# Optimization experiments

Hardware: AMD Instinct MI355X
Metric: run time of the kernel (lower is better)

Reference implementation:

```python
import jax, jax.numpy as jnp
import numpy as np

B, F0, D = 2048, 39, 16
LAYER_SIZES = [128, 128, 128]  # split_half=True -> field_nums [39, 64, 64]


def setup_inputs() -> dict:
    key = jax.random.key(0)
    ks = jax.random.split(key, 1 + 2 * len(LAYER_SIZES))
    inputs = jax.random.normal(ks[0], (B, F0, D), dtype=jnp.float32)
    out = {"inputs": inputs}
    field_nums = [F0]
    for i, size in enumerate(LAYER_SIZES):
        fk = field_nums[-1]
        fan_in = F0 * fk  # conv1d filter fan-in (kernel width 1)
        scale = np.sqrt(2.0 / (fan_in + size)).astype(np.float32)  # glorot
        # filter stored as [F0, Fk, size]; TF flat index is h0*Fk + hk
        out[f"w{i}"] = jax.random.normal(ks[1 + 2 * i], (F0, fk, size), dtype=jnp.float32) * scale
        out[f"b{i}"] = jnp.zeros((size,), dtype=jnp.float32)
        field_nums.append(size // 2)  # split_half=True
    return out


def reference(inputs, w0, w1, w2, b0, b1, b2):
    # CIN: per-embedding-dim outer product of x0 and x_{k-1}, then 1x1 conv
    # (shared dense over field pairs). Fused here as a single einsum per layer.
    x0 = inputs  # [B, F0, D]
    xk = inputs  # [B, Fk, D]
    params = [(w0, b0), (w1, b1), (w2, b2)]
    n_layers = len(params)
    direct = []
    for idx, (W, b) in enumerate(params):
        # out[b, s, d] = sum_{h,k} x0[b,h,d] * xk[b,k,d] * W[h,k,s]
        z = jnp.einsum('bhd,bkd,hks->bsd', x0, xk, W) + b[None, :, None]
        z = jax.nn.relu(z)  # activation='relu'
        if idx != n_layers - 1:
            half = z.shape[1] // 2  # split_half: first half feeds next layer
            xk = z[:, :half, :]
            direct.append(z[:, half:, :])
        else:
            direct.append(z)
    logit = jnp.sum(jnp.concatenate(direct, axis=1), axis=-1)  # [B, 64+64+128]
    return logit
```

## Files before the change

### kernel.cpp

```cpp
#include <hip/hip_runtime.h>
#include <stdint.h>
#include <stddef.h>

#define F0N  39
#define SN   128
#define NB   8
#define X0TS 45
#define XKTS 72
#define WBLK 8192
#define NHB2 234

typedef __attribute__((ext_vector_type(8))) short short8;
typedef __attribute__((ext_vector_type(4))) float floatx4;

__device__ __forceinline__ uint16_t f2bf(float f) {
  uint32_t u = __float_as_uint(f);
  u += 0x7fffu + ((u >> 16) & 1u);
  return (uint16_t)(u >> 16);
}

__global__ __launch_bounds__(256) void cin_prepass(
    const float* __restrict__ w0, const float* __restrict__ w1,
    const float* __restrict__ w2, uint16_t* __restrict__ wt) {
  __shared__ float T[32 * 132];
  const int bc = blockIdx.x;
  const int ch = bc & 1;
  const int lh = bc >> 1;
  const int L = lh / F0N;
  const int h = lh - L * F0N;
  const float* W = (L == 0) ? w0 : ((L == 1) ? w1 : w2);
  const int fk = (L == 0) ? 39 : 64;
  const int tid = threadIdx.x;

  for (int e = tid; e < 4096; e += 256) {
    int kc = e >> 7, s = e & 127;
    int k = ch * 32 + kc;
    T[kc * 132 + s] = (k < fk) ? W[(h * fk + k) * SN + s] : 0.0f;
  }
  __syncthreads();
  uint32_t* dst = (uint32_t*)(wt + (size_t)lh * WBLK);
  for (int i = tid; i < 2048; i += 256) {
    int st = i >> 8, w = i & 255;
    int ln = w >> 2, jp = w & 3;
    int quad = ln >> 4, l16 = ln & 15;
    int k0 = quad * 8 + jp * 2;
    int s = st * 16 + l16;
    dst[(size_t)(st * 2 + ch) * 256 + w] =
        (uint32_t)f2bf(T[k0 * 132 + s]) | ((uint32_t)f2bf(T[(k0 + 1) * 132 + s]) << 16);
  }
}

__global__ __launch_bounds__(1024) void cin_main(
    const float* __restrict__ x,
    const float* __restrict__ bias0, const float* __restrict__ bias1,
    const float* __restrict__ bias2,
    const uint16_t* __restrict__ wt,
    float* __restrict__ out) {

  __shared__ __align__(16) float    X0T[NB * 16 * X0TS];
  __shared__ __align__(16) uint16_t XKT[NB * 16 * XKTS];

  const int tid  = threadIdx.x;
  const int lane = tid & 63;
  const int wave = tid >> 6;
  const int st   = wave >> 1;
  const int bg   = wave & 1;
  const int l16  = lane & 15;
  const int quad = lane >> 4;
  const int bbase = blockIdx.x * NB;

  {
    float* p = X0T;
#pragma unroll
    for (int i = 0; i < 6; i++) { int e = tid + 1024 * i; if (e < NB * 16 * X0TS) p[e] = 0.f; }
    uint32_t* q = (uint32_t*)XKT;
#pragma unroll
    for (int i = 0; i < 5; i++) { int e = tid + 1024 * i; if (e < NB * 16 * XKTS / 2) q[e] = 0u; }
  }
  __syncthreads();

#pragma unroll
  for (int it = 0; it < 5; ++it) {
    int e = tid + it * 1024;
    if (e < NB * F0N * 16) {
      float v = x[(size_t)bbase * (F0N * 16) + e];
      int d = e & 15, p = e >> 4;
      int b = p / F0N, h = p - b * F0N;
      X0T[(b * 16 + d) * X0TS + h] = v;
    }
  }
  __syncthreads();

  if (tid < 512) {
    int b = tid >> 6, d = (tid >> 2) & 15, kg = tid & 3;
    const float* src = &X0T[(b * 16 + d) * X0TS];
    uint32_t* drow = (uint32_t*)&XKT[(b * 16 + d) * XKTS + kg * 16];
#pragma unroll
    for (int i2 = 0; i2 < 8; i2++) {
      int k0 = kg * 16 + i2 * 2;
      uint32_t lo = (k0 < 39)     ? (uint32_t)f2bf(src[k0])     : 0u;
      uint32_t hi = (k0 + 1 < 39) ? (uint32_t)f2bf(src[k0 + 1]) : 0u;
      drow[i2] = lo | (hi << 16);
    }
  }
  __syncthreads();

  const int stlane = st * 1024 + lane * 8;

  short8 Wc0 = *(const short8*)(wt + stlane);
  short8 Wc1 = *(const short8*)(wt + stlane + 512);

  int ih = 0;
#pragma unroll 1
  for (int L = 0; L < 3; ++L) {
    short8 Bf0[4], Bf1[4];
#pragma unroll
    for (int bi = 0; bi < 4; ++bi) {
      const uint16_t* r = XKT + ((bg * 4 + bi) * 16 + l16) * XKTS + quad * 8;
      Bf0[bi] = *(const short8*)r;
      Bf1[bi] = *(const short8*)(r + 32);
    }

    floatx4 z[4] = {};
    const floatx4 zero4 = {0.f, 0.f, 0.f, 0.f};

#pragma unroll 3
    for (int h = 0; h < 39; ++h, ++ih) {
      int ihn = ih + 1;
      if (ihn > 116) ihn = 116;
      const uint16_t* wb = wt + (size_t)ihn * WBLK + stlane;
      short8 Wn0 = *(const short8*)(wb);
      short8 Wn1 = *(const short8*)(wb + 512);

      float xs[4];
#pragma unroll
      for (int bi = 0; bi < 4; ++bi)
        xs[bi] = X0T[((bg * 4 + bi) * 16 + l16) * X0TS + h];

#pragma unroll
      for (int bi = 0; bi < 4; ++bi) {
        floatx4 y = __builtin_amdgcn_mfma_f32_16x16x32_bf16(Wc0, Bf0[bi], zero4, 0, 0, 0);
        y = __builtin_amdgcn_mfma_f32_16x16x32_bf16(Wc1, Bf1[bi], y, 0, 0, 0);
#pragma unroll
        for (int r = 0; r < 4; ++r) z[bi][r] += xs[bi] * y[r];
      }
      Wc0 = Wn0;
      Wc1 = Wn1;
    }

    const float* bp = (L == 0) ? bias0 : ((L == 1) ? bias1 : bias2);
#pragma unroll
    for (int bi = 0; bi < 4; ++bi) {
      const int b = bg * 4 + bi;
#pragma unroll
      for (int r = 0; r < 4; ++r) {
        float t = fmaxf(z[bi][r] + bp[st * 16 + quad * 4 + r], 0.f);
        if (L < 2 && st < 4)
          XKT[(b * 16 + l16) * XKTS + st * 16 + quad * 4 + r] = f2bf(t);
        float s4 = t;
        s4 += __shfl_xor(s4, 1);
        s4 += __shfl_xor(s4, 2);
        s4 += __shfl_xor(s4, 4);
        s4 += __shfl_xor(s4, 8);
        if (l16 == 0) {
          int s = st * 16 + quad * 4 + r;
          if (L == 2)       out[(size_t)(bbase + b) * 256 + 128 + s] = s4;
          else if (s >= 64) out[(size_t)(bbase + b) * 256 + L * 64 + (s - 64)] = s4;
        }
      }
    }
    if (L < 2) __syncthreads();
  }
}

extern "C" void kernel_launch(void* const* d_in, const int* in_sizes, int n_in,
                              void* d_out, int out_size, void* d_ws, size_t ws_size,
                              hipStream_t stream) {
  (void)in_sizes; (void)n_in; (void)out_size; (void)ws_size;
  const float* x  = (const float*)d_in[0];
  const float* w0 = (const float*)d_in[1];
  const float* b0 = (const float*)d_in[2];
  const float* w1 = (const float*)d_in[3];
  const float* b1 = (const float*)d_in[4];
  const float* w2 = (const float*)d_in[5];
  const float* b2 = (const float*)d_in[6];
  uint16_t* wt    = (uint16_t*)d_ws;

  cin_prepass<<<NHB2, 256, 0, stream>>>(w0, w1, w2, wt);
  cin_main<<<256, 1024, 0, stream>>>(x, b0, b1, b2, wt, (float*)d_out);
}
```

Before: 138.0 us.

## Premultiply x0 into bf16 operand tiles and accumulate directly in MFMA

Instead of running two MFMAs per h into a zero accumulator and then scaling by x0 on the CUDA cores, each h step builds a bf16 tile U = x0[h]*xk in shared memory, double-buffered across h, and feeds it to MFMA that accumulates straight into z. The goal is to remove the per-h scalar FMA epilogue and keep the reduction over h inside the matrix cores. In exchange it adds shared-memory tile construction, LDS reads, a __syncthreads per h, and an extra bf16 rounding of the product. The xk layout is changed to fit the MFMA operand format, and dynamic shared memory is enlarged to hold the two U buffers.

Result: slower. 149.8 us (+8.5%).

```diff
diff --git a/kernel.cpp b/kernel.cpp
--- a/kernel.cpp
+++ b/kernel.cpp
@@ -6,17 +6,36 @@
 #define SN   128
 #define NB   8
 #define X0TS 45
-#define XKTS 72
 #define WBLK 8192
 #define NHB2 234
+#define X0T_BYTES 23040
+#define XKT_OFF   23040
+#define U0_OFF    39424
+#define U1_OFF    55808
+#define SMEM_TOTAL 72192
 
 typedef __attribute__((ext_vector_type(8))) short short8;
 typedef __attribute__((ext_vector_type(4))) float floatx4;
+typedef __attribute__((ext_vector_type(8))) float floatx8;
+typedef __attribute__((ext_vector_type(8))) __bf16 bf16x8;
 
 __device__ __forceinline__ uint16_t f2bf(float f) {
   uint32_t u = __float_as_uint(f);
   u += 0x7fffu + ((u >> 16) & 1u);
   return (uint16_t)(u >> 16);
+}
+
+__device__ __forceinline__ void build_u(const float* X0T, const uint16_t* XKT,
+                                        uint16_t* dst, int xrow, int toff, int hn) {
+  float xs = X0T[xrow + hn];
+  short8 xkv = *(const short8*)(XKT + toff);
+  bf16x8 xb = __builtin_bit_cast(bf16x8, xkv);
+  floatx8 xf = __builtin_convertvector(xb, floatx8);
+  floatx8 pf;
+#pragma unroll
+  for (int j = 0; j < 8; ++j) pf[j] = xf[j] * xs;
+  *(short8*)(dst + toff) =
+      __builtin_bit_cast(short8, __builtin_convertvector(pf, bf16x8));
 }
 
 __global__ __launch_bounds__(256) void cin_prepass(
@@ -57,8 +76,11 @@
     const uint16_t* __restrict__ wt,
     float* __restrict__ out) {
 
-  __shared__ __align__(16) float    X0T[NB * 16 * X0TS];
-  __shared__ __align__(16) uint16_t XKT[NB * 16 * XKTS];
+  extern __shared__ __align__(16) char smem[];
+  float*    X0T = (float*)smem;
+  uint16_t* XKT = (uint16_t*)(smem + XKT_OFF);
+  uint16_t* U0  = (uint16_t*)(smem + U0_OFF);
+  uint16_t* U1  = (uint16_t*)(smem + U1_OFF);
 
   const int tid  = threadIdx.x;
   const int lane = tid & 63;
@@ -69,13 +91,12 @@
   const int quad = lane >> 4;
   const int bbase = blockIdx.x * NB;
 
+  const int xrow = ((tid >> 7) * 16 + (tid & 15)) * X0TS;
+  const int toff = tid * 8;
+
   {
-    float* p = X0T;
-#pragma unroll
-    for (int i = 0; i < 6; i++) { int e = tid + 1024 * i; if (e < NB * 16 * X0TS) p[e] = 0.f; }
-    uint32_t* q = (uint32_t*)XKT;
-#pragma unroll
-    for (int i = 0; i < 5; i++) { int e = tid + 1024 * i; if (e < NB * 16 * XKTS / 2) q[e] = 0u; }
+#pragma unroll
+    for (int i = 0; i < 6; i++) { int e = tid + 1024 * i; if (e < NB * 16 * X0TS) X0T[e] = 0.f; }
   }
   __syncthreads();
 
@@ -91,21 +112,20 @@
   }
   __syncthreads();
 
-  if (tid < 512) {
-    int b = tid >> 6, d = (tid >> 2) & 15, kg = tid & 3;
-    const float* src = &X0T[(b * 16 + d) * X0TS];
-    uint32_t* drow = (uint32_t*)&XKT[(b * 16 + d) * XKTS + kg * 16];
-#pragma unroll
-    for (int i2 = 0; i2 < 8; i2++) {
-      int k0 = kg * 16 + i2 * 2;
-      uint32_t lo = (k0 < 39)     ? (uint32_t)f2bf(src[k0])     : 0u;
-      uint32_t hi = (k0 + 1 < 39) ? (uint32_t)f2bf(src[k0 + 1]) : 0u;
-      drow[i2] = lo | (hi << 16);
-    }
+  {
+    int k8 = (tid >> 4) & 7;
+    uint16_t vals[8];
+#pragma unroll
+    for (int j = 0; j < 8; ++j) {
+      int k = k8 * 8 + j;
+      vals[j] = (k < F0N) ? f2bf(X0T[xrow + k]) : (uint16_t)0;
+    }
+    *(short8*)(XKT + toff) = *(short8*)vals;
   }
   __syncthreads();
 
   const int stlane = st * 1024 + lane * 8;
+  const int ulane = bg * 4096 + quad * 128 + l16 * 8;
 
   short8 Wc0 = *(const short8*)(wt + stlane);
   short8 Wc1 = *(const short8*)(wt + stlane + 512);
@@ -113,18 +133,15 @@
   int ih = 0;
 #pragma unroll 1
   for (int L = 0; L < 3; ++L) {
-    short8 Bf0[4], Bf1[4];
-#pragma unroll
-    for (int bi = 0; bi < 4; ++bi) {
-      const uint16_t* r = XKT + ((bg * 4 + bi) * 16 + l16) * XKTS + quad * 8;
-      Bf0[bi] = *(const short8*)r;
-      Bf1[bi] = *(const short8*)(r + 32);
-    }
+    uint16_t* ua  = U0;
+    uint16_t* ubn = U1;
+
+    build_u(X0T, XKT, ua, xrow, toff, 0);
+    __syncthreads();
 
     floatx4 z[4] = {};
-    const floatx4 zero4 = {0.f, 0.f, 0.f, 0.f};
-
-#pragma unroll 3
+
+#pragma unroll 1
     for (int h = 0; h < 39; ++h, ++ih) {
       int ihn = ih + 1;
       if (ihn > 116) ihn = 116;
@@ -132,20 +149,20 @@
       short8 Wn0 = *(const short8*)(wb);
       short8 Wn1 = *(const short8*)(wb + 512);
 
-      float xs[4];
-#pragma unroll
-      for (int bi = 0; bi < 4; ++bi)
-        xs[bi] = X0T[((bg * 4 + bi) * 16 + l16) * X0TS + h];
+      build_u(X0T, XKT, ubn, xrow, toff, h + 1);
 
 #pragma unroll
       for (int bi = 0; bi < 4; ++bi) {
-        floatx4 y = __builtin_amdgcn_mfma_f32_16x16x32_bf16(Wc0, Bf0[bi], zero4, 0, 0, 0);
-        y = __builtin_amdgcn_mfma_f32_16x16x32_bf16(Wc1, Bf1[bi], y, 0, 0, 0);
-#pragma unroll
-        for (int r = 0; r < 4; ++r) z[bi][r] += xs[bi] * y[r];
+        const uint16_t* ur = ua + ulane + bi * 1024;
+        short8 u0 = *(const short8*)(ur);
+        short8 u1 = *(const short8*)(ur + 512);
+        z[bi] = __builtin_amdgcn_mfma_f32_16x16x32_bf16(Wc0, u0, z[bi], 0, 0, 0);
+        z[bi] = __builtin_amdgcn_mfma_f32_16x16x32_bf16(Wc1, u1, z[bi], 0, 0, 0);
       }
       Wc0 = Wn0;
       Wc1 = Wn1;
+      { uint16_t* t = ua; ua = ubn; ubn = t; }
+      __syncthreads();
     }
 
     const float* bp = (L == 0) ? bias0 : ((L == 1) ? bias1 : bias2);
@@ -155,8 +172,10 @@
 #pragma unroll
       for (int r = 0; r < 4; ++r) {
         float t = fmaxf(z[bi][r] + bp[st * 16 + quad * 4 + r], 0.f);
-        if (L < 2 && st < 4)
-          XKT[(b * 16 + l16) * XKTS + st * 16 + quad * 4 + r] = f2bf(t);
+        if (L < 2 && st < 4) {
+          int s = st * 16 + quad * 4 + r;
+          XKT[((b * 8 + (s >> 3)) * 16 + l16) * 8 + (s & 7)] = f2bf(t);
+        }
         float s4 = t;
         s4 += __shfl_xor(s4, 1);
         s4 += __shfl_xor(s4, 2);
@@ -186,6 +205,14 @@
   const float* b2 = (const float*)d_in[6];
   uint16_t* wt    = (uint16_t*)d_ws;
 
+  static bool smem_cfg = false;
+  if (!smem_cfg) {
+    (void)hipFuncSetAttribute((const void*)cin_main,
+                              hipFuncAttributeMaxDynamicSharedMemorySize,
+                              SMEM_TOTAL);
+    smem_cfg = true;
+  }
+
   cin_prepass<<<NHB2, 256, 0, stream>>>(w0, w1, w2, wt);
-  cin_main<<<256, 1024, 0, stream>>>(x, b0, b1, b2, wt, (float*)d_out);
-}
+  cin_main<<<256, 1024, SMEM_TOTAL, stream>>>(x, b0, b1, b2, wt, (float*)d_out);
+}
```

## Software-pipeline MFMA results across h iterations and use packed FMA combine

Applied to the files above, without the earlier changes.

Restructures the h loop so the MFMA chain for iteration h is issued before the scaling/accumulation of iteration h-1's results. This hides MFMA latency behind the VALU combine step. It also switches the combine to 2-wide float vectors so the compiler can emit packed FMA, and hoists the X0T row offsets out of the loop. The cost is extra registers for the in-flight results, which could add pressure in a 1024-thread block.

New measurement: 142.2 us. 3.0% more time.

```diff
diff --git a/kernel.cpp b/kernel.cpp
--- a/kernel.cpp
+++ b/kernel.cpp
@@ -12,6 +12,7 @@
 
 typedef __attribute__((ext_vector_type(8))) short short8;
 typedef __attribute__((ext_vector_type(4))) float floatx4;
+typedef __attribute__((ext_vector_type(2))) float floatx2;
 
 __device__ __forceinline__ uint16_t f2bf(float f) {
   uint32_t u = __float_as_uint(f);
@@ -107,8 +108,25 @@
 
   const int stlane = st * 1024 + lane * 8;
 
+  int xoff[4];
+#pragma unroll
+  for (int bi = 0; bi < 4; ++bi)
+    xoff[bi] = ((bg * 4 + bi) * 16 + l16) * X0TS;
+
   short8 Wc0 = *(const short8*)(wt + stlane);
   short8 Wc1 = *(const short8*)(wt + stlane + 512);
+
+#define YCHAIN(DST, BI)                                                       \
+    floatx4 DST = __builtin_amdgcn_mfma_f32_16x16x32_bf16(Wc0, Bf0[BI], zero4, 0, 0, 0); \
+    DST = __builtin_amdgcn_mfma_f32_16x16x32_bf16(Wc1, Bf1[BI], DST, 0, 0, 0);
+#define COMBINE(ZI, YP, XS)                                                   \
+    {                                                                         \
+      floatx2 xv = {(XS), (XS)};                                              \
+      floatx2* zp = (floatx2*)&z[ZI];                                         \
+      const floatx2* yq = (const floatx2*)&(YP);                              \
+      zp[0] += xv * yq[0];                                                    \
+      zp[1] += xv * yq[1];                                                    \
+    }
 
   int ih = 0;
 #pragma unroll 1
@@ -124,29 +142,56 @@
     floatx4 z[4] = {};
     const floatx4 zero4 = {0.f, 0.f, 0.f, 0.f};
 
-#pragma unroll 3
-    for (int h = 0; h < 39; ++h, ++ih) {
+    floatx4 yp0, yp1, yp2, yp3;
+    float xsp[4];
+    {
+      const uint16_t* wb = wt + (size_t)(ih + 1) * WBLK + stlane;
+      short8 Wn0 = *(const short8*)(wb);
+      short8 Wn1 = *(const short8*)(wb + 512);
+#pragma unroll
+      for (int bi = 0; bi < 4; ++bi) xsp[bi] = X0T[xoff[bi]];
+      YCHAIN(t0, 0) yp0 = t0;
+      YCHAIN(t1, 1) yp1 = t1;
+      YCHAIN(t2, 2) yp2 = t2;
+      YCHAIN(t3, 3) yp3 = t3;
+      Wc0 = Wn0;
+      Wc1 = Wn1;
+      ++ih;
+    }
+
+#pragma unroll 2
+    for (int h = 1; h < 39; ++h, ++ih) {
       int ihn = ih + 1;
       if (ihn > 116) ihn = 116;
       const uint16_t* wb = wt + (size_t)ihn * WBLK + stlane;
       short8 Wn0 = *(const short8*)(wb);
       short8 Wn1 = *(const short8*)(wb + 512);
 
-      float xs[4];
-#pragma unroll
-      for (int bi = 0; bi < 4; ++bi)
-        xs[bi] = X0T[((bg * 4 + bi) * 16 + l16) * X0TS + h];
-
-#pragma unroll
-      for (int bi = 0; bi < 4; ++bi) {
-        floatx4 y = __builtin_amdgcn_mfma_f32_16x16x32_bf16(Wc0, Bf0[bi], zero4, 0, 0, 0);
-        y = __builtin_amdgcn_mfma_f32_16x16x32_bf16(Wc1, Bf1[bi], y, 0, 0, 0);
-#pragma unroll
-        for (int r = 0; r < 4; ++r) z[bi][r] += xs[bi] * y[r];
-      }
+      float xsc[4];
+#pragma unroll
+      for (int bi = 0; bi < 4; ++bi) xsc[bi] = X0T[xoff[bi] + h];
+
+      YCHAIN(yc0, 0)
+      YCHAIN(yc1, 1)
+      YCHAIN(yc2, 2)
+      YCHAIN(yc3, 3)
+
+      COMBINE(0, yp0, xsp[0])
+      COMBINE(1, yp1, xsp[1])
+      COMBINE(2, yp2, xsp[2])
+      COMBINE(3, yp3, xsp[3])
+
+      yp0 = yc0; yp1 = yc1; yp2 = yc2; yp3 = yc3;
+#pragma unroll
+      for (int bi = 0; bi < 4; ++bi) xsp[bi] = xsc[bi];
       Wc0 = Wn0;
       Wc1 = Wn1;
     }
+
+    COMBINE(0, yp0, xsp[0])
+    COMBINE(1, yp1, xsp[1])
+    COMBINE(2, yp2, xsp[2])
+    COMBINE(3, yp3, xsp[3])
 
     const float* bp = (L == 0) ? bias0 : ((L == 1) ? bias1 : bias2);
 #pragma unroll
@@ -171,6 +216,8 @@
     }
     if (L < 2) __syncthreads();
   }
+#undef YCHAIN
+#undef COMBINE
 }
 
 extern "C" void kernel_launch(void* const* d_in, const int* in_sizes, int n_in,
```
